# Optimization experiments

Measured on AMD Instinct MI355X. Metric: run time of the kernel, lower is better.

The kernel has to match this reference:

```python
import jax, jax.numpy as jnp
import numpy as np

B, T, D = 4, 2048, 384
MIN_DUR = 8.0
W_SCALE = 0.02  # keeps softplus output < 8 so clamped+rounded durations are exactly 8


def setup_inputs() -> dict:
    key = jax.random.key(0)
    k_x, k_w1, k_w2 = jax.random.split(key, 3)
    x = jax.random.normal(k_x, (B, T, D), dtype=jnp.float32)
    w1 = jax.random.normal(k_w1, (D, D // 2), dtype=jnp.float32) * W_SCALE
    b1 = jnp.zeros((D // 2,), dtype=jnp.float32)
    w2 = jax.random.normal(k_w2, (D // 2, 1), dtype=jnp.float32) * W_SCALE
    b2 = jnp.zeros((1,), dtype=jnp.float32)
    total_length = B * T * int(MIN_DUR)  # == duration_pred.sum() by construction (all durs clamp to 8)
    return {"x": x, "w1": w1, "b1": b1, "w2": w2, "b2": b2, "total_length": total_length}


def reference(x, w1, b1, w2, b2, total_length):
    # 2-layer MLP duration predictor: Linear -> ReLU -> Linear -> Softplus, squeeze(-1)
    h = jax.nn.relu(jnp.einsum("btd,dh->bth", x, w1) + b1)
    duration_pred = jax.nn.softplus(jnp.einsum("bth,ho->bto", h, w2) + b2)[..., 0]  # (B, T)
    # inference path: clamp to min duration then round
    duration_pred = jnp.round(jnp.maximum(duration_pred, MIN_DUR))
    # Original expands using batch-0 durations for all rows (faithful to source).
    dur0 = duration_pred[0].astype(jnp.int32)            # (T,)
    cum = jnp.cumsum(dur0)                               # (T,) end offsets
    pos = jnp.arange(total_length)                       # static output length
    idx = jnp.minimum(jnp.searchsorted(cum, pos, side="right"), x.shape[1] - 1)
    valid = pos < cum[-1]
    # parallel gather replacing the per-timestep slice-assign loop; zeros past total fill
    expanded = jnp.where(valid[None, :, None], x[:, idx, :], jnp.zeros((), x.dtype))
    return expanded, duration_pred
```

## Files before the change

### kernel.cpp

```cpp
#include <hip/hip_runtime.h>
#include <hip/hip_bf16.h>
#include <math.h>

#define BB 4
#define TT 2048
#define DD 384
#define HH 192
#define TOTAL_LEN 65536
#define EXP_ELEMS (BB * TOTAL_LEN * DD)
#define F4_PER_ROW (DD / 4)
#define TOTAL_F4 (BB * TOTAL_LEN * F4_PER_ROW)

__global__ __launch_bounds__(256) void mlp_dur_kernel(
    const float* __restrict__ x, const float* __restrict__ w1,
    const float* __restrict__ b1, const float* __restrict__ w2,
    const float* __restrict__ b2, float* __restrict__ dur_out,
    int* __restrict__ dur0) {
  const int lane = threadIdx.x & 63;
  const int wave = __builtin_amdgcn_readfirstlane(threadIdx.x >> 6);
  const int row0 = (blockIdx.x * 4 + wave) * 8;
  const int j0 = lane, j1 = lane + 64, j2 = lane + 128;

  float acc[8][3];
#pragma unroll
  for (int r = 0; r < 8; ++r) {
    acc[r][0] = 0.f; acc[r][1] = 0.f; acc[r][2] = 0.f;
  }

  for (int k = 0; k < DD; k += 4) {
    float wa[4], wb[4], wc[4];
#pragma unroll
    for (int kk = 0; kk < 4; ++kk) {
      const float* wrow = w1 + (size_t)(k + kk) * HH;
      wa[kk] = wrow[j0];
      wb[kk] = wrow[j1];
      wc[kk] = wrow[j2];
    }
#pragma unroll
    for (int r = 0; r < 8; ++r) {
      const float* xrow = x + (size_t)(row0 + r) * DD + k;
#pragma unroll
      for (int kk = 0; kk < 4; ++kk) {
        const float xv = xrow[kk];
        acc[r][0] = fmaf(xv, wa[kk], acc[r][0]);
        acc[r][1] = fmaf(xv, wb[kk], acc[r][1]);
        acc[r][2] = fmaf(xv, wc[kk], acc[r][2]);
      }
    }
  }

  const float b10 = b1[j0], b11 = b1[j1], b12 = b1[j2];
  const float w20 = w2[j0], w21 = w2[j1], w22 = w2[j2];
  const float bias2 = b2[0];

#pragma unroll
  for (int r = 0; r < 8; ++r) {
    float s = fmaxf(acc[r][0] + b10, 0.f) * w20 +
              fmaxf(acc[r][1] + b11, 0.f) * w21 +
              fmaxf(acc[r][2] + b12, 0.f) * w22;
#pragma unroll
    for (int off = 32; off > 0; off >>= 1) s += __shfl_down(s, off, 64);
    if (lane == 0) {
      const float z = s + bias2;
      const float sp = fmaxf(z, 0.f) + log1pf(expf(-fabsf(z)));
      const float dur = rintf(fmaxf(sp, 8.0f));
      const int row = row0 + r;
      dur_out[row] = dur;
      if (row < TT) dur0[row] = (int)dur;
    }
  }
}

__global__ __launch_bounds__(256) void scan_kernel(const int* __restrict__ dur0,
                                                   int* __restrict__ cum) {
  __shared__ int lds[256];
  const int tid = threadIdx.x;
  const int base = tid * 8;
  int v[8];
  int run = 0;
#pragma unroll
  for (int i = 0; i < 8; ++i) {
    run += dur0[base + i];
    v[i] = run;
  }
  lds[tid] = run;
  __syncthreads();
  for (int off = 1; off < 256; off <<= 1) {
    const int t = (tid >= off) ? lds[tid - off] : 0;
    __syncthreads();
    lds[tid] += t;
    __syncthreads();
  }
  const int excl = lds[tid] - run;
#pragma unroll
  for (int i = 0; i < 8; ++i) cum[base + i] = v[i] + excl;
}

__global__ __launch_bounds__(256) void idx_kernel(const int* __restrict__ cum,
                                                  int* __restrict__ idx_map) {
  const int pos = blockIdx.x * 256 + threadIdx.x;
  const int total = cum[TT - 1];
  int lo = 0, hi = TT - 1;
  while (lo < hi) {
    const int mid = (lo + hi) >> 1;
    if (cum[mid] > pos) hi = mid;
    else lo = mid + 1;
  }
  idx_map[pos] = (pos < total) ? lo : -1;
}

__global__ __launch_bounds__(256) void expand_kernel(
    const float4* __restrict__ x4, const int* __restrict__ idx_map,
    float4* __restrict__ out4) {
  const unsigned t = blockIdx.x * 256u + threadIdx.x;
  const unsigned row = t / 96u;
  const unsigned col = t - row * 96u;
  const unsigned b = row >> 16;
  const unsigned pos = row & 65535u;
  const int id = idx_map[pos];
  float4 v = {0.f, 0.f, 0.f, 0.f};
  if (id >= 0) v = x4[((size_t)b * TT + (unsigned)id) * F4_PER_ROW + col];
  out4[t] = v;
}

extern "C" void kernel_launch(void* const* d_in, const int* in_sizes, int n_in,
                              void* d_out, int out_size, void* d_ws,
                              size_t ws_size, hipStream_t stream) {
  const float* x = (const float*)d_in[0];
  const float* w1 = (const float*)d_in[1];
  const float* b1 = (const float*)d_in[2];
  const float* w2 = (const float*)d_in[3];
  const float* b2 = (const float*)d_in[4];

  float* out = (float*)d_out;
  float* dur_out = out + (size_t)EXP_ELEMS;

  int* ws = (int*)d_ws;
  int* dur0 = ws;
  int* cum = ws + TT;
  int* idx_map = ws + 2 * TT;

  mlp_dur_kernel<<<256, 256, 0, stream>>>(x, w1, b1, w2, b2, dur_out, dur0);
  scan_kernel<<<1, 256, 0, stream>>>(dur0, cum);
  idx_kernel<<<TOTAL_LEN / 256, 256, 0, stream>>>(cum, idx_map);
  expand_kernel<<<TOTAL_F4 / 256, 256, 0, stream>>>((const float4*)x, idx_map,
                                                    (float4*)out);
}
```

Before: 471.7 us.

## Stage MLP input rows in LDS and use nontemporal stores in expand

Result: faster. 452.0 us (-4.2%).

```diff
diff --git a/kernel.cpp b/kernel.cpp
--- a/kernel.cpp
+++ b/kernel.cpp
@@ -10,64 +10,68 @@
 #define EXP_ELEMS (BB * TOTAL_LEN * DD)
 #define F4_PER_ROW (DD / 4)
 #define TOTAL_F4 (BB * TOTAL_LEN * F4_PER_ROW)
+#define ROWS_PER_BLK 16
+
+typedef float f32x4 __attribute__((ext_vector_type(4)));
 
 __global__ __launch_bounds__(256) void mlp_dur_kernel(
     const float* __restrict__ x, const float* __restrict__ w1,
     const float* __restrict__ b1, const float* __restrict__ w2,
     const float* __restrict__ b2, float* __restrict__ dur_out,
     int* __restrict__ dur0) {
-  const int lane = threadIdx.x & 63;
-  const int wave = __builtin_amdgcn_readfirstlane(threadIdx.x >> 6);
-  const int row0 = (blockIdx.x * 4 + wave) * 8;
-  const int j0 = lane, j1 = lane + 64, j2 = lane + 128;
+  __shared__ float xs[ROWS_PER_BLK * DD];
+  __shared__ float part[ROWS_PER_BLK * 4];
 
-  float acc[8][3];
+  const int tid = threadIdx.x;
+  const int lane = tid & 63;
+  const int wave = tid >> 6;
+  const int row0 = blockIdx.x * ROWS_PER_BLK;
+
+  const f32x4* xg = (const f32x4*)(x + (size_t)row0 * DD);
+  f32x4* xs4 = (f32x4*)xs;
 #pragma unroll
-  for (int r = 0; r < 8; ++r) {
-    acc[r][0] = 0.f; acc[r][1] = 0.f; acc[r][2] = 0.f;
-  }
+  for (int i = 0; i < 6; ++i) xs4[i * 256 + tid] = xg[i * 256 + tid];
+  __syncthreads();
 
-  for (int k = 0; k < DD; k += 4) {
-    float wa[4], wb[4], wc[4];
+  float acc[ROWS_PER_BLK];
 #pragma unroll
-    for (int kk = 0; kk < 4; ++kk) {
-      const float* wrow = w1 + (size_t)(k + kk) * HH;
-      wa[kk] = wrow[j0];
-      wb[kk] = wrow[j1];
-      wc[kk] = wrow[j2];
-    }
+  for (int r = 0; r < ROWS_PER_BLK; ++r) acc[r] = 0.f;
+
+  const int j = tid;
+  if (j < HH) {
+    for (int k = 0; k < DD; k += 4) {
+      float w[4];
 #pragma unroll
-    for (int r = 0; r < 8; ++r) {
-      const float* xrow = x + (size_t)(row0 + r) * DD + k;
+      for (int kk = 0; kk < 4; ++kk) w[kk] = w1[(size_t)(k + kk) * HH + j];
 #pragma unroll
-      for (int kk = 0; kk < 4; ++kk) {
-        const float xv = xrow[kk];
-        acc[r][0] = fmaf(xv, wa[kk], acc[r][0]);
-        acc[r][1] = fmaf(xv, wb[kk], acc[r][1]);
-        acc[r][2] = fmaf(xv, wc[kk], acc[r][2]);
+      for (int r = 0; r < ROWS_PER_BLK; ++r) {
+        const float* xr = xs + r * DD + k;
+#pragma unroll
+        for (int kk = 0; kk < 4; ++kk) acc[r] = fmaf(xr[kk], w[kk], acc[r]);
       }
     }
   }
 
-  const float b10 = b1[j0], b11 = b1[j1], b12 = b1[j2];
-  const float w20 = w2[j0], w21 = w2[j1], w22 = w2[j2];
-  const float bias2 = b2[0];
+  const float b1v = (j < HH) ? b1[j] : 0.f;
+  const float w2v = (j < HH) ? w2[j] : 0.f;
 
 #pragma unroll
-  for (int r = 0; r < 8; ++r) {
-    float s = fmaxf(acc[r][0] + b10, 0.f) * w20 +
-              fmaxf(acc[r][1] + b11, 0.f) * w21 +
-              fmaxf(acc[r][2] + b12, 0.f) * w22;
+  for (int r = 0; r < ROWS_PER_BLK; ++r) {
+    float s = fmaxf(acc[r] + b1v, 0.f) * w2v;
 #pragma unroll
     for (int off = 32; off > 0; off >>= 1) s += __shfl_down(s, off, 64);
-    if (lane == 0) {
-      const float z = s + bias2;
-      const float sp = fmaxf(z, 0.f) + log1pf(expf(-fabsf(z)));
-      const float dur = rintf(fmaxf(sp, 8.0f));
-      const int row = row0 + r;
-      dur_out[row] = dur;
-      if (row < TT) dur0[row] = (int)dur;
-    }
+    if (lane == 0) part[r * 4 + wave] = s;
+  }
+  __syncthreads();
+
+  if (tid < ROWS_PER_BLK) {
+    const float z = part[tid * 4] + part[tid * 4 + 1] + part[tid * 4 + 2] +
+                    part[tid * 4 + 3] + b2[0];
+    const float sp = fmaxf(z, 0.f) + log1pf(expf(-fabsf(z)));
+    const float dur = rintf(fmaxf(sp, 8.0f));
+    const int row = row0 + tid;
+    dur_out[row] = dur;
+    if (row < TT) dur0[row] = (int)dur;
   }
 }
 
@@ -110,17 +114,17 @@
 }
 
 __global__ __launch_bounds__(256) void expand_kernel(
-    const float4* __restrict__ x4, const int* __restrict__ idx_map,
-    float4* __restrict__ out4) {
+    const f32x4* __restrict__ x4, const int* __restrict__ idx_map,
+    f32x4* __restrict__ out4) {
   const unsigned t = blockIdx.x * 256u + threadIdx.x;
   const unsigned row = t / 96u;
   const unsigned col = t - row * 96u;
   const unsigned b = row >> 16;
   const unsigned pos = row & 65535u;
   const int id = idx_map[pos];
-  float4 v = {0.f, 0.f, 0.f, 0.f};
+  f32x4 v = {0.f, 0.f, 0.f, 0.f};
   if (id >= 0) v = x4[((size_t)b * TT + (unsigned)id) * F4_PER_ROW + col];
-  out4[t] = v;
+  __builtin_nontemporal_store(v, out4 + t);
 }
 
 extern "C" void kernel_launch(void* const* d_in, const int* in_sizes, int n_in,
@@ -140,9 +144,9 @@
   int* cum = ws + TT;
   int* idx_map = ws + 2 * TT;
 
-  mlp_dur_kernel<<<256, 256, 0, stream>>>(x, w1, b1, w2, b2, dur_out, dur0);
+  mlp_dur_kernel<<<512, 256, 0, stream>>>(x, w1, b1, w2, b2, dur_out, dur0);
   scan_kernel<<<1, 256, 0, stream>>>(dur0, cum);
   idx_kernel<<<TOTAL_LEN / 256, 256, 0, stream>>>(cum, idx_map);
-  expand_kernel<<<TOTAL_F4 / 256, 256, 0, stream>>>((const float4*)x, idx_map,
-                                                    (float4*)out);
+  expand_kernel<<<TOTAL_F4 / 256, 256, 0, stream>>>((const f32x4*)x, idx_map,
+                                                    (f32x4*)out);
 }
```
